# Optimization experiments

Hardware: AMD Instinct MI355X
Metric: run time of the kernel (lower is better)

Reference implementation:

```python
import jax, jax.numpy as jnp
import numpy as np

B, C, Himg, Wimg = 8, 256, 128, 128
KC, VC, HID = 256, 256, 1024


def _conv(x, w, b, pad, groups=1):
    y = jax.lax.conv_general_dilated(
        x, w, (1, 1), [(pad[0], pad[0]), (pad[1], pad[1])],
        dimension_numbers=('NCHW', 'OIHW', 'NCHW'), feature_group_count=groups)
    return y + b[None, :, None, None]


def _ln(x, g, b, eps=1e-5):
    m = x.mean(-1, keepdims=True)
    v = ((x - m) ** 2).mean(-1, keepdims=True)
    return (x - m) / jnp.sqrt(v + eps) * g + b


def setup_inputs() -> dict:
    key = jax.random.key(0)
    ks = jax.random.split(key, 24)
    s = 0.02
    inp = {
        'x': jax.random.normal(ks[0], (B, C, Himg, Wimg), jnp.float32),
        'H': Himg, 'W': Wimg,
        # directional K/Q convs: dir0 kernel (1,3), dir1 kernel (3,1)
        'wk1': s * jax.random.normal(ks[1], (KC, C, 1, 3), jnp.float32),
        'bk1': jnp.zeros((KC,), jnp.float32),
        'wk2': s * jax.random.normal(ks[2], (KC, C, 3, 1), jnp.float32),
        'bk2': jnp.zeros((KC,), jnp.float32),
        'wq1': s * jax.random.normal(ks[3], (KC, C, 1, 3), jnp.float32),
        'bq1': jnp.zeros((KC,), jnp.float32),
        'wq2': s * jax.random.normal(ks[4], (KC, C, 3, 1), jnp.float32),
        'bq2': jnp.zeros((KC,), jnp.float32),
        'wv': s * jax.random.normal(ks[5], (VC, C, 1, 1), jnp.float32),
        'bv': jnp.zeros((VC,), jnp.float32),
        'wr': s * jax.random.normal(ks[6], (C, 2 * VC, 1, 1), jnp.float32),
        'br': jnp.zeros((C,), jnp.float32),
        'g1': jnp.ones((C,), jnp.float32), 'b1': jnp.zeros((C,), jnp.float32),
        'g2': jnp.ones((C,), jnp.float32), 'b2': jnp.zeros((C,), jnp.float32),
        'w_fc1': s * jax.random.normal(ks[7], (HID, C), jnp.float32),
        'b_fc1': jnp.zeros((HID,), jnp.float32),
        'w_dw': s * jax.random.normal(ks[8], (HID, 1, 3, 3), jnp.float32),
        'b_dw': jnp.zeros((HID,), jnp.float32),
        'w_fc2': s * jax.random.normal(ks[9], (C, HID), jnp.float32),
        'b_fc2': jnp.zeros((C,), jnp.float32),
    }
    return inp


def reference(x, H, W, wk1, bk1, wk2, bk2, wq1, bq1, wq2, bq2, wv, bv, wr, br,
              g1, b1, g2, b2, w_fc1, b_fc1, w_dw, b_dw, w_fc2, b_fc2):
    b, c, h, w = x.shape
    N = h * w
    xseq = x.reshape(b, c, N).transpose(0, 2, 1)          # b N c
    n1 = _ln(xseq, g1, b1)
    xn = n1.transpose(0, 2, 1).reshape(b, c, h, w)

    val = _conv(xn, wv, bv, (0, 0)).reshape(b, VC, N)     # b vc n
    attended, maps = [], []
    ctx = None
    for (wk, bk, wq, bq, pad) in [(wk1, bk1, wq1, bq1, (0, 1)),
                                  (wk2, bk2, wq2, bq2, (1, 0))]:
        k = _conv(xn, wk, bk, pad).reshape(b, KC, N)
        q = _conv(xn, wq, bq, pad).reshape(b, KC, N)
        key_s = jax.nn.softmax(k, axis=2)                 # softmax over spatial
        qry_s = jax.nn.softmax(q, axis=1)                 # softmax over channels
        ctx = jnp.einsum('bkn,bvn->bkv', key_s, val)      # O(n) linear attention
        av = jnp.einsum('bkv,bkn->bvn', ctx, qry_s).reshape(b, VC, h, w)
        attended.append(av)
        maps.append(key_s.mean(axis=1).reshape(b, h, w))
    agg = jnp.concatenate(attended, axis=1)               # b 2vc h w
    attn = _conv(agg, wr, br, (0, 0))                     # b c h w
    amap = jnp.stack(maps, axis=0).mean(axis=0)

    tx = xseq + attn.reshape(b, c, N).transpose(0, 2, 1)  # residual
    n2 = _ln(tx, g2, b2)
    h1 = n2 @ w_fc1.T + b_fc1                             # b N 4c
    h1img = h1.transpose(0, 2, 1).reshape(b, HID, h, w)
    dw = _conv(h1img, w_dw, b_dw, (1, 1), groups=HID)
    a = jax.nn.gelu(dw.reshape(b, HID, N).transpose(0, 2, 1), approximate=False)
    ffn = a @ w_fc2.T + b_fc2
    mx = (tx + ffn).transpose(0, 2, 1).reshape(b, c, h, w)
    return (mx, ctx, amap)
```

## Files before the change

kernel.cpp:

```cpp
#include <hip/hip_runtime.h>
#include <hip/hip_bf16.h>

#define B_ 8
#define C_ 256
#define H_ 128
#define W_ 128
#define N_ 16384
#define KC_ 256
#define VC_ 256
#define HID_ 1024

typedef unsigned short ushort_t;
typedef __bf16 bf16x8 __attribute__((ext_vector_type(8)));
typedef float f32x4 __attribute__((ext_vector_type(4)));
typedef ushort_t u16x8 __attribute__((ext_vector_type(8)));

static __device__ __forceinline__ ushort_t f2bu(float f) {
  __hip_bfloat16 h = __float2bfloat16(f);
  return *reinterpret_cast<ushort_t*>(&h);
}
static __device__ __forceinline__ float bu2f(ushort_t u) {
  __hip_bfloat16 h;
  *reinterpret_cast<ushort_t*>(&h) = u;
  return __bfloat162float(h);
}

#define GLD16(gp, lp) __builtin_amdgcn_global_load_lds( \
    (const __attribute__((address_space(1))) void*)(gp), \
    (__attribute__((address_space(3))) void*)(lp), 16, 0, 0)

__global__ __launch_bounds__(256) void pack_all(
    const float* __restrict__ wk1, const float* __restrict__ wk2,
    const float* __restrict__ wq1, const float* __restrict__ wq2,
    const float* __restrict__ wv, const float* __restrict__ wfc1,
    const float* __restrict__ wfc2, const float* __restrict__ wdw,
    const float* __restrict__ bk1, const float* __restrict__ bk2,
    const float* __restrict__ bq1, const float* __restrict__ bq2,
    const float* __restrict__ bv, const float* __restrict__ wr,
    ushort_t* __restrict__ zbuf,
    float* __restrict__ bKV, float* __restrict__ bQ, float* __restrict__ wdwT,
    ushort_t* __restrict__ wvp, ushort_t* __restrict__ wfc1p,
    ushort_t* __restrict__ wfc2p, ushort_t* __restrict__ wrp,
    ushort_t* __restrict__ wkkp, ushort_t* __restrict__ wqqp) {
  int idx = blockIdx.x * 256 + threadIdx.x;
  const int MC = KC_ * C_;
  if (idx < 512) {
    zbuf[idx] = 0;
    bQ[idx] = (idx < 256) ? bq1[idx] : bq2[idx - 256];
    return;
  }
  idx -= 512;
  if (idx < 768) {
    bKV[idx] = (idx < 256) ? bk1[idx] : (idx < 512 ? bk2[idx - 256] : bv[idx - 512]);
    return;
  }
  idx -= 768;
  if (idx < 9216) { int c = idx / 9, t = idx % 9; wdwT[t * HID_ + c] = wdw[idx]; return; }
  idx -= 9216;
  if (idx < VC_ * C_) { wvp[idx] = f2bu(wv[idx]); return; }
  idx -= VC_ * C_;
  if (idx < HID_ * C_) { wfc1p[idx] = f2bu(wfc1[idx]); return; }
  idx -= HID_ * C_;
  if (idx < C_ * HID_) { wfc2p[idx] = f2bu(wfc2[idx]); return; }
  idx -= C_ * HID_;
  if (idx < C_ * 512) { wrp[idx] = f2bu(wr[idx]); return; }
  idx -= C_ * 512;
  if (idx < MC) {
    #pragma unroll
    for (int t = 0; t < 3; ++t) wkkp[t * MC + idx] = f2bu(wk1[idx * 3 + t]);
    return;
  }
  idx -= MC;
  if (idx < MC) {
    #pragma unroll
    for (int t = 0; t < 3; ++t) wkkp[3 * MC + t * MC + idx] = f2bu(wk2[idx * 3 + t]);
    return;
  }
  idx -= MC;
  if (idx < MC) {
    #pragma unroll
    for (int t = 0; t < 3; ++t) wqqp[t * MC + idx] = f2bu(wq1[idx * 3 + t]);
    return;
  }
  idx -= MC;
  if (idx < MC) {
    #pragma unroll
    for (int t = 0; t < 3; ++t) wqqp[3 * MC + t * MC + idx] = f2bu(wq2[idx * 3 + t]);
    return;
  }
}

__global__ __launch_bounds__(256) void ln1t_kernel(const float* __restrict__ x,
    const float* __restrict__ g, const float* __restrict__ beta,
    ushort_t* __restrict__ out) {
  __shared__ float T[256][67];
  __shared__ float st[2][4][64];
  __shared__ float mr[64], rs[64];
  int z = blockIdx.z;
  int n0 = blockIdx.x * 64;
  int t = threadIdx.x;
  const float* xb = x + (size_t)z * C_ * N_;
  #pragma unroll
  for (int j = 0; j < 16; ++j) {
    int e = (j * 256 + t) * 4;
    int c = e >> 6, n = e & 63;
    float4 v = *(const float4*)&xb[(size_t)c * N_ + n0 + n];
    T[c][n] = v.x; T[c][n + 1] = v.y; T[c][n + 2] = v.z; T[c][n + 3] = v.w;
  }
  __syncthreads();
  {
    int n = t & 63, part = t >> 6;
    float s1 = 0.f, s2 = 0.f;
    for (int c = part * 64; c < part * 64 + 64; ++c) { float v = T[c][n]; s1 += v; s2 += v * v; }
    st[0][part][n] = s1; st[1][part][n] = s2;
  }
  __syncthreads();
  if (t < 64) {
    float s1 = st[0][0][t] + st[0][1][t] + st[0][2][t] + st[0][3][t];
    float s2 = st[1][0][t] + st[1][1][t] + st[1][2][t] + st[1][3][t];
    float m = s1 * (1.f / C_);
    float v = s2 * (1.f / C_) - m * m;
    mr[t] = m; rs[t] = rsqrtf(v + 1e-5f);
  }
  __syncthreads();
  {
    int n = t >> 2, cc = (t & 3) * 64;
    float m = mr[n], r = rs[n];
    ushort_t* po = out + (size_t)z * N_ * C_ + (size_t)(n0 + n) * C_ + cc;
    #pragma unroll
    for (int j0 = 0; j0 < 64; j0 += 8) {
      u16x8 o;
      #pragma unroll
      for (int j = 0; j < 8; ++j) {
        int c = cc + j0 + j;
        o[j] = f2bu((T[c][n] - m) * r * g[c] + beta[c]);
      }
      *(u16x8*)(po + j0) = o;
    }
  }
}

__global__ __launch_bounds__(256) void ln2t_kernel(const ushort_t* __restrict__ x,
    const float* __restrict__ g, const float* __restrict__ beta,
    ushort_t* __restrict__ out) {
  __shared__ ushort_t T[256][72];
  __shared__ float st[2][4][64];
  __shared__ float mr[64], rs[64];
  int z = blockIdx.z;
  int n0 = blockIdx.x * 64;
  int t = threadIdx.x;
  const ushort_t* xb = x + (size_t)z * C_ * N_;
  #pragma unroll
  for (int j = 0; j < 8; ++j) {
    int e = (j * 256 + t) * 8;
    int c = e >> 6, n = e & 63;
    *(u16x8*)&T[c][n] = *(const u16x8*)&xb[(size_t)c * N_ + n0 + n];
  }
  __syncthreads();
  {
    int n = t & 63, part = t >> 6;
    float s1 = 0.f, s2 = 0.f;
    for (int c = part * 64; c < part * 64 + 64; ++c) { float v = bu2f(T[c][n]); s1 += v; s2 += v * v; }
    st[0][part][n] = s1; st[1][part][n] = s2;
  }
  __syncthreads();
  if (t < 64) {
    float s1 = st[0][0][t] + st[0][1][t] + st[0][2][t] + st[0][3][t];
    float s2 = st[1][0][t] + st[1][1][t] + st[1][2][t] + st[1][3][t];
    float m = s1 * (1.f / C_);
    float v = s2 * (1.f / C_) - m * m;
    mr[t] = m; rs[t] = rsqrtf(v + 1e-5f);
  }
  __syncthreads();
  {
    int n = t >> 2, cc = (t & 3) * 64;
    float m = mr[n], r = rs[n];
    ushort_t* po = out + (size_t)z * N_ * C_ + (size_t)(n0 + n) * C_ + cc;
    #pragma unroll
    for (int j0 = 0; j0 < 64; j0 += 8) {
      u16x8 o;
      #pragma unroll
      for (int j = 0; j < 8; ++j) {
        int c = cc + j0 + j;
        o[j] = f2bu((bu2f(T[c][n]) - m) * r * g[c] + beta[c]);
      }
      *(u16x8*)(po + j0) = o;
    }
  }
}

template<int TAPS, int DIMSEL, int OMODE, int SPLIT, bool BDUAL, bool BSOFT>
__global__ __launch_bounds__(256) void mfma_gemm(
    const ushort_t* __restrict__ A, long Abatch, int lda, long Aplane, long Adirstride,
    const ushort_t* __restrict__ B, const ushort_t* __restrict__ B2, long Bbatch, int ldb,
    const float* __restrict__ bias,
    const float* __restrict__ resF, const ushort_t* __restrict__ resB, long Resbatch,
    float* __restrict__ outF, ushort_t* __restrict__ outB, ushort_t* __restrict__ outB2,
    ushort_t* __restrict__ outB3,
    long Outbatch, int ldo, int Ksteps, const ushort_t* __restrict__ zbuf,
    const float2* __restrict__ qstats) {
  __shared__ ushort_t sm[17408];
  int tid = threadIdx.x;
  int bx = blockIdx.x, by = blockIdx.y, bz = blockIdx.z;
  if (gridDim.x == 128) bx = ((bx & 7) << 4) | (bx >> 3);
  int b = bz / SPLIT, sK = bz % SPLIT;
  long koff = (long)sK * Ksteps * 64;
  int dsel = (DIMSEL == 3) ? (by < 2 ? 1 : 2)
           : (DIMSEL == 4) ? (by < 2 ? 1 : (by < 4 ? 2 : 0))
           : DIMSEL;
  int m0 = (DIMSEL == 3 || DIMSEL == 4) ? ((by & 1) * 128) : (by * 128);
  int bofs = (DIMSEL == 3 || DIMSEL == 4) ? ((by >> 1) * 256) : 0;
  const ushort_t* Ab = A + (size_t)b * Abatch + koff
      + ((DIMSEL == 3 || DIMSEL == 4) ? (long)(by >> 1) * Adirstride : 0L);
  const ushort_t* Bb = B + (size_t)b * Bbatch + (BDUAL ? 0 : koff);
  const ushort_t* B2b = BDUAL ? (B2 + (size_t)b * Bbatch) : nullptr;
  int n0 = bx * 128;
  int lane = tid & 63, wid = tid >> 6, wm = wid >> 1, wn = wid & 1;

  f32x4 acc[4][4];
  #pragma unroll
  for (int i = 0; i < 4; i++)
    #pragma unroll
    for (int j = 0; j < 4; j++) acc[i][j] = (f32x4)0.f;

  for (int t = 0; t < TAPS; ++t) {
    if (TAPS == 3 && dsel == 2) {
      if ((bx == 0 && t == 0) || (bx == H_ - 1 && t == 2)) continue;
    }
    if (DIMSEL == 4 && dsel == 0 && t != 1) continue;
    const ushort_t* At = Ab + ((DIMSEL == 4 && dsel == 0) ? 0L : (long)t * Aplane);
    for (int ks = 0; ks < Ksteps; ++ks) {
      int k0 = ks * 64;
      #pragma unroll
      for (int i = 0; i < 4; i++) {
        int s = tid + i * 256;
        int row = s >> 3, pc = s & 7;
        int lc = pc ^ (row & 7);
        const ushort_t* g = At + (long)(m0 + row) * lda + k0 + lc * 8;
        GLD16(g, &sm[s * 8]);
      }
      if (BDUAL && BSOFT) {
        int dir = (ks < Ksteps / 2) ? 0 : 1;
        const ushort_t* Bsel = dir ? B2b : Bb;
        int kb = (ks - dir * (Ksteps / 2)) * 64;
        #pragma unroll
        for (int i = 0; i < 4; i++) {
          int s = tid + i * 256;
          int row = s >> 3, pc = s & 7;
          int lc = pc ^ (row & 7);
          u16x8 e = *(const u16x8*)(Bsel + (long)(n0 + row) * ldb + kb + lc * 8);
          float2 st = qstats[(size_t)dir * B_ * N_ + (size_t)bz * N_ + n0 + row];
          u16x8 o;
          #pragma unroll
          for (int j = 0; j < 8; j++)
            o[j] = f2bu(__expf(bu2f(e[j]) - st.x) * st.y);
          *(u16x8*)&sm[8192 + s * 8] = o;
        }
      } else {
        #pragma unroll
        for (int i = 0; i < 4; i++) {
          int s = tid + i * 256;
          int row = s >> 3, pc = s & 7;
          int lc = pc ^ (row & 7);
          const ushort_t* g;
          if (BDUAL) {
            const ushort_t* Bsel = (ks < Ksteps / 2) ? Bb : B2b;
            int kb = ((ks < Ksteps / 2) ? ks : ks - Ksteps / 2) * 64;
            g = Bsel + (long)(n0 + row) * ldb + kb + lc * 8;
          } else if (TAPS == 3 && dsel == 1) {
            int wpos = row + (t - 1);
            if (0 <= wpos && wpos < W_)
              g = Bb + (long)(n0 + row + (t - 1)) * ldb + k0 + lc * 8;
            else
              g = zbuf;
          } else if (TAPS == 3 && dsel == 2) {
            g = Bb + (long)(n0 + row + (t - 1) * W_) * ldb + k0 + lc * 8;
          } else {
            g = Bb + (long)(n0 + row) * ldb + k0 + lc * 8;
          }
          GLD16(g, &sm[8192 + s * 8]);
        }
      }
      __syncthreads();
      #pragma unroll
      for (int kk = 0; kk < 2; kk++) {
        bf16x8 av[4], bv[4];
        int r16 = lane & 15;
        int sl = (lane >> 4) + kk * 4;
        #pragma unroll
        for (int fm = 0; fm < 4; fm++) {
          int row = wm * 64 + fm * 16 + r16;
          av[fm] = *(const bf16x8*)&sm[row * 64 + ((sl ^ (row & 7)) * 8)];
        }
        #pragma unroll
        for (int fn = 0; fn < 4; fn++) {
          int row = wn * 64 + fn * 16 + r16;
          bv[fn] = *(const bf16x8*)&sm[8192 + row * 64 + ((sl ^ (row & 7)) * 8)];
        }
        #pragma unroll
        for (int fm = 0; fm < 4; fm++)
          #pragma unroll
          for (int fn = 0; fn < 4; fn++)
            acc[fm][fn] = __builtin_amdgcn_mfma_f32_16x16x32_bf16(av[fm], bv[fn], acc[fm][fn], 0, 0, 0);
      }
      __syncthreads();
    }
  }

  int r16 = lane & 15, rq = lane >> 4;
  if (OMODE == 1 || OMODE == 2 || OMODE == 7) {
    ushort_t* obase;
    if (DIMSEL == 3 || DIMSEL == 4)
      obase = (blockIdx.y >= 4) ? outB3 : (blockIdx.y >= 2 ? outB2 : outB);
    else
      obase = outB;
    ushort_t* ob = obase + (size_t)bz * Outbatch;
    #pragma unroll
    for (int fm = 0; fm < 4; fm++) {
      #pragma unroll
      for (int fn = 0; fn < 4; fn++) {
        int lm = wm * 64 + fm * 16 + rq * 4;
        int ln = wn * 64 + fn * 16 + r16;
        f32x4 a = acc[fm][fn];
        if (OMODE == 2) {
          #pragma unroll
          for (int r = 0; r < 4; r++)
            sm[ln * 136 + lm + r] = f2bu(a[r] + bias[bofs + m0 + lm + r]);
        } else {
          #pragma unroll
          for (int r = 0; r < 4; r++)
            sm[(lm + r) * 136 + ln] = f2bu(a[r] + bias[bofs + m0 + lm + r]);
        }
      }
    }
    __syncthreads();
    int row = tid >> 1, half = (tid & 1) * 64;
    const ushort_t* src = &sm[row * 136 + half];
    if (OMODE == 7) {
      const float* xb = resF + (size_t)bz * Resbatch + (size_t)(m0 + row) * ldo + n0 + half;
      ushort_t* dst = &ob[(size_t)(m0 + row) * ldo + n0 + half];
      #pragma unroll
      for (int j = 0; j < 8; j++) {
        u16x8 v = *(const u16x8*)(src + j * 8);
        float4 x0 = *(const float4*)(xb + j * 8);
        float4 x1 = *(const float4*)(xb + j * 8 + 4);
        u16x8 o;
        o[0] = f2bu(bu2f(v[0]) + x0.x); o[1] = f2bu(bu2f(v[1]) + x0.y);
        o[2] = f2bu(bu2f(v[2]) + x0.z); o[3] = f2bu(bu2f(v[3]) + x0.w);
        o[4] = f2bu(bu2f(v[4]) + x1.x); o[5] = f2bu(bu2f(v[5]) + x1.y);
        o[6] = f2bu(bu2f(v[6]) + x1.z); o[7] = f2bu(bu2f(v[7]) + x1.w);
        *(u16x8*)(dst + j * 8) = o;
      }
    } else {
      ushort_t* dst;
      if (OMODE == 1) dst = &ob[(size_t)(m0 + row) * ldo + n0 + half];
      else            dst = &ob[(size_t)(n0 + row) * ldo + m0 + half];
      #pragma unroll
      for (int j = 0; j < 8; j++)
        *(u16x8*)(dst + j * 8) = *(const u16x8*)(src + j * 8);
    }
  } else {
    #pragma unroll
    for (int fm = 0; fm < 4; fm++) {
      #pragma unroll
      for (int fn = 0; fn < 4; fn++) {
        int mrow = m0 + wm * 64 + fm * 16 + rq * 4;
        int ncol = n0 + wn * 64 + fn * 16 + r16;
        f32x4 a = acc[fm][fn];
        if (OMODE == 6) {
          float* of = outF + (size_t)bz * Outbatch;
          #pragma unroll
          for (int r = 0; r < 4; r++)
            of[(size_t)(mrow + r) * ldo + ncol] = a[r];
        } else if (OMODE == 8) {
          float* of = outF + (size_t)bz * Outbatch;
          const ushort_t* rp = resB + (size_t)bz * Resbatch;
          #pragma unroll
          for (int r = 0; r < 4; r++) {
            size_t o = (size_t)(mrow + r) * ldo + ncol;
            of[o] = a[r] + bias[mrow + r] + bu2f(rp[o]);
          }
        }
      }
    }
  }
}

__global__ __launch_bounds__(256) void softmax_spatial2(ushort_t* __restrict__ p0,
                                                        ushort_t* __restrict__ p1) {
  int r = blockIdx.x;
  ushort_t* p = (r < B_ * KC_) ? (p0 + (size_t)r * N_) : (p1 + (size_t)(r - B_ * KC_) * N_);
  int tid = threadIdx.x;
  __shared__ float red[256];
  u16x8 v[8];
  #pragma unroll
  for (int j = 0; j < 8; j++) v[j] = *(const u16x8*)&p[tid * 8 + j * 2048];
  float mx = -1e30f;
  #pragma unroll
  for (int j = 0; j < 8; j++)
    #pragma unroll
    for (int e = 0; e < 8; e++) mx = fmaxf(mx, bu2f(v[j][e]));
  red[tid] = mx; __syncthreads();
  for (int s = 128; s > 0; s >>= 1) { if (tid < s) red[tid] = fmaxf(red[tid], red[tid + s]); __syncthreads(); }
  mx = red[0]; __syncthreads();
  float sum = 0.f;
  #pragma unroll
  for (int j = 0; j < 8; j++)
    #pragma unroll
    for (int e = 0; e < 8; e++) sum += __expf(bu2f(v[j][e]) - mx);
  red[tid] = sum; __syncthreads();
  for (int s = 128; s > 0; s >>= 1) { if (tid < s) red[tid] += red[tid + s]; __syncthreads(); }
  float inv = 1.f / red[0];
  #pragma unroll
  for (int j = 0; j < 8; j++) {
    u16x8 o;
    #pragma unroll
    for (int e = 0; e < 8; e++) o[e] = f2bu(__expf(bu2f(v[j][e]) - mx) * inv);
    *(u16x8*)&p[tid * 8 + j * 2048] = o;
  }
}

__global__ __launch_bounds__(256) void chstats_kernel(const ushort_t* __restrict__ p0,
                                                      const ushort_t* __restrict__ p1,
                                                      float2* __restrict__ qstats) {
  int tid = threadIdx.x;
  size_t rowg = (size_t)blockIdx.x * 32 + (tid >> 3);
  int part = tid & 7;
  const ushort_t* q = (rowg < (size_t)B_ * N_) ? (p0 + rowg * KC_)
                                               : (p1 + (rowg - (size_t)B_ * N_) * KC_);
  u16x8 v[4];
  #pragma unroll
  for (int j = 0; j < 4; j++) v[j] = *(const u16x8*)&q[part * 8 + j * 64];
  float mx = -1e30f;
  #pragma unroll
  for (int j = 0; j < 4; j++)
    #pragma unroll
    for (int e = 0; e < 8; e++) mx = fmaxf(mx, bu2f(v[j][e]));
  mx = fmaxf(mx, __shfl_xor(mx, 1));
  mx = fmaxf(mx, __shfl_xor(mx, 2));
  mx = fmaxf(mx, __shfl_xor(mx, 4));
  float sum = 0.f;
  #pragma unroll
  for (int j = 0; j < 4; j++)
    #pragma unroll
    for (int e = 0; e < 8; e++) sum += __expf(bu2f(v[j][e]) - mx);
  sum += __shfl_xor(sum, 1);
  sum += __shfl_xor(sum, 2);
  sum += __shfl_xor(sum, 4);
  if (part == 0) qstats[rowg] = make_float2(mx, 1.f / sum);
}

__global__ __launch_bounds__(256) void amap2_kernel(const ushort_t* __restrict__ k0,
    const ushort_t* __restrict__ k1, float* __restrict__ amap) {
  __shared__ float red[256][8];
  int tid = threadIdx.x;
  int ngrp = tid & 63, part = tid >> 6;
  int nblock = blockIdx.x * 512;
  int b = nblock >> 14;
  int n = (nblock & 16383) + ngrp * 8;
  const ushort_t* b0 = k0 + (size_t)b * KC_ * N_ + n;
  const ushort_t* b1 = k1 + (size_t)b * KC_ * N_ + n;
  float s[8];
  #pragma unroll
  for (int j = 0; j < 8; j++) s[j] = 0.f;
  for (int c = part * 64; c < part * 64 + 64; ++c) {
    u16x8 a = *(const u16x8*)&b0[(size_t)c * N_];
    u16x8 d = *(const u16x8*)&b1[(size_t)c * N_];
    #pragma unroll
    for (int j = 0; j < 8; j++) s[j] += bu2f(a[j]) + bu2f(d[j]);
  }
  #pragma unroll
  for (int j = 0; j < 8; j++) red[tid][j] = s[j];
  __syncthreads();
  if (tid < 64) {
    float t[8];
    #pragma unroll
    for (int j = 0; j < 8; j++)
      t[j] = (red[tid][j] + red[tid + 64][j] + red[tid + 128][j] + red[tid + 192][j])
             * (1.f / (2.f * KC_));
    float* dst = amap + (size_t)nblock + tid * 8;
    *(float4*)dst = make_float4(t[0], t[1], t[2], t[3]);
    *(float4*)(dst + 4) = make_float4(t[4], t[5], t[6], t[7]);
  }
}

template<bool F32OUT>
__global__ __launch_bounds__(256) void ctx_reduce(const float* __restrict__ part,
                                                  float* __restrict__ outF,
                                                  ushort_t* __restrict__ outB, int split) {
  int idx = blockIdx.x * 256 + threadIdx.x;
  int b = idx >> 16;
  int r = idx & 65535;
  float s = 0.f;
  for (int k = 0; k < split; k++)
    s += part[((size_t)(b * split + k)) * KC_ * VC_ + r];
  if (F32OUT) outF[idx] = s;
  outB[idx] = f2bu(s);
}

__global__ __launch_bounds__(256) void dwgelu_t(const ushort_t* __restrict__ h1t,
    const float* __restrict__ wdwT, const float* __restrict__ bdw,
    ushort_t* __restrict__ actT) {
  const ushort_t* h1 = h1t + (size_t)blockIdx.y * N_ * HID_;
  ushort_t* act = actT + (size_t)blockIdx.y * N_ * HID_;
  int pix = blockIdx.x * 2 + (threadIdx.x >> 7);
  int c = (threadIdx.x & 127) * 8;
  int h = pix >> 7, w = pix & 127;
  float s[8];
  {
    float4 b0 = *(const float4*)&bdw[c];
    float4 b1 = *(const float4*)&bdw[c + 4];
    s[0]=b0.x; s[1]=b0.y; s[2]=b0.z; s[3]=b0.w;
    s[4]=b1.x; s[5]=b1.y; s[6]=b1.z; s[7]=b1.w;
  }
  #pragma unroll
  for (int di = -1; di <= 1; ++di) {
    int h2 = h + di;
    if ((unsigned)h2 >= H_) continue;
    #pragma unroll
    for (int dj = -1; dj <= 1; ++dj) {
      int w2 = w + dj;
      if ((unsigned)w2 >= W_) continue;
      int tap = (di + 1) * 3 + (dj + 1);
      u16x8 v = *(const u16x8*)&h1[(size_t)(h2 * W_ + w2) * HID_ + c];
      const float* wp = &wdwT[tap * HID_ + c];
      float4 w0 = *(const float4*)wp, w1 = *(const float4*)(wp + 4);
      s[0] += w0.x * bu2f(v[0]); s[1] += w0.y * bu2f(v[1]);
      s[2] += w0.z * bu2f(v[2]); s[3] += w0.w * bu2f(v[3]);
      s[4] += w1.x * bu2f(v[4]); s[5] += w1.y * bu2f(v[5]);
      s[6] += w1.z * bu2f(v[6]); s[7] += w1.w * bu2f(v[7]);
    }
  }
  u16x8 o;
  #pragma unroll
  for (int j = 0; j < 8; j++) {
    float gl = 0.5f * s[j] * (1.f + erff(s[j] * 0.70710678118654752f));
    o[j] = f2bu(gl);
  }
  *(u16x8*)&act[(size_t)pix * HID_ + c] = o;
}

extern "C" void kernel_launch(void* const* d_in, const int* in_sizes, int n_in,
                              void* d_out, int out_size, void* d_ws, size_t ws_size,
                              hipStream_t stream) {
  const float* x    = (const float*)d_in[0];
  const float* wk1  = (const float*)d_in[3];
  const float* bk1  = (const float*)d_in[4];
  const float* wk2  = (const float*)d_in[5];
  const float* bk2  = (const float*)d_in[6];
  const float* wq1  = (const float*)d_in[7];
  const float* bq1  = (const float*)d_in[8];
  const float* wq2  = (const float*)d_in[9];
  const float* bq2  = (const float*)d_in[10];
  const float* wv   = (const float*)d_in[11];
  const float* bv   = (const float*)d_in[12];
  const float* wr   = (const float*)d_in[13];
  const float* br   = (const float*)d_in[14];
  const float* g1   = (const float*)d_in[15];
  const float* b1   = (const float*)d_in[16];
  const float* g2   = (const float*)d_in[17];
  const float* b2   = (const float*)d_in[18];
  const float* wfc1 = (const float*)d_in[19];
  const float* bfc1 = (const float*)d_in[20];
  const float* wdw  = (const float*)d_in[21];
  const float* bdw  = (const float*)d_in[22];
  const float* wfc2 = (const float*)d_in[23];
  const float* bfc2 = (const float*)d_in[24];

  const size_t big = (size_t)B_ * C_ * N_;
  const long  CN  = (long)C_ * N_;
  const long  NC2 = (long)N_ * C_;
  const long  NH  = (long)N_ * HID_;
  const int   MC  = KC_ * C_;

  uint8_t* w8 = (uint8_t*)d_ws;
  size_t off = 0;
  ushort_t* xnt  = (ushort_t*)(w8 + off); off += 67108864;
  ushort_t* kq   = (ushort_t*)(w8 + off); off += 67108864;
  ushort_t* Mbuf = (ushort_t*)(w8 + off); off += (size_t)B_ * C_ * 512 * 2;
  ushort_t* wkkp = (ushort_t*)(w8 + off); off += 6 * MC * 2;
  ushort_t* wvp  = (ushort_t*)(w8 + off); off += MC * 2;
  ushort_t* wqqp = (ushort_t*)(w8 + off); off += 6 * MC * 2;
  ushort_t* wfc1p= (ushort_t*)(w8 + off); off += HID_ * C_ * 2;
  ushort_t* wfc2p= (ushort_t*)(w8 + off); off += C_ * HID_ * 2;
  float* wdwT    = (float*)(w8 + off);    off += 9 * HID_ * 4;
  float* bKV     = (float*)(w8 + off);    off += 768 * 4;
  float* bQ      = (float*)(w8 + off);    off += 512 * 4;
  ushort_t* wrp  = (ushort_t*)(w8 + off); off += C_ * 512 * 2;
  ushort_t* ctx0b= (ushort_t*)(w8 + off); off += (size_t)B_ * KC_ * VC_ * 2;
  ushort_t* ctx1b= (ushort_t*)(w8 + off); off += (size_t)B_ * KC_ * VC_ * 2;
  float2* qstats = (float2*)(w8 + off);   off += (size_t)2 * B_ * N_ * 8;
  ushort_t* zbuf = (ushort_t*)(w8 + off); off += 1024;
  const size_t partBytes = (size_t)8 * B_ * KC_ * VC_ * 4;
  size_t need_pair = off + 67108864 + partBytes;
  size_t need8 = off + partBytes;
  size_t need4 = off + partBytes / 2;
  int csplit; bool pairFFN = false;
  ushort_t* actX = nullptr;
  float* part;
  if (ws_size >= need_pair) {
    pairFFN = true; csplit = 8;
    actX = (ushort_t*)(w8 + off);
    part = (float*)(w8 + off + 67108864);
  } else if (ws_size >= need8) {
    csplit = 8; part = (float*)(w8 + off);
  } else if (ws_size >= need4) {
    csplit = 4; part = (float*)(w8 + off);
  } else return;
  const float* fzero = (const float*)zbuf;

  float* mx_out   = (float*)d_out;
  float* ctx_out  = mx_out + big;
  float* amap_out = ctx_out + (size_t)B_ * KC_ * VC_;

  ushort_t* mxlo = (ushort_t*)d_out;
  ushort_t* mxhi = (ushort_t*)d_out + big;

  ushort_t* txn  = xnt;

  dim3 blk(256);

  pack_all<<<3881, blk, 0, stream>>>(wk1, wk2, wq1, wq2, wv, wfc1, wfc2, wdw,
                                     bk1, bk2, bq1, bq2, bv, wr,
                                     zbuf, bKV, bQ, wdwT,
                                     wvp, wfc1p, wfc2p, wrp, wkkp, wqqp);

  ln1t_kernel<<<dim3(N_ / 64, 1, B_), blk, 0, stream>>>(x, g1, b1, xnt);

  mfma_gemm<3, 4, 1, 1, false, false><<<dim3(N_ / 128, 6, B_), blk, 0, stream>>>(
      wkkp, 0, C_, (long)MC, (long)3 * MC, xnt, nullptr, NC2, C_,
      bKV, nullptr, nullptr, 0,
      nullptr, kq, mxhi, mxlo, (long)KC_ * N_, N_, C_ / 64, zbuf, nullptr);

  softmax_spatial2<<<2 * B_ * KC_, blk, 0, stream>>>(kq, mxhi);
  amap2_kernel<<<B_ * N_ / 512, blk, 0, stream>>>(kq, mxhi, amap_out);

  for (int d = 0; d < 2; ++d) {
    const ushort_t* Ksrc = d ? mxhi : kq;
    if (csplit == 8)
      mfma_gemm<1, 0, 6, 8, false, false><<<dim3(VC_ / 128, KC_ / 128, B_ * 8), blk, 0, stream>>>(
          Ksrc, (long)KC_ * N_, N_, 0, 0, mxlo, nullptr, (long)VC_ * N_, N_,
          nullptr, nullptr, nullptr, 0,
          part, nullptr, nullptr, nullptr, (long)KC_ * VC_, VC_, (N_ / 8) / 64, zbuf, nullptr);
    else
      mfma_gemm<1, 0, 6, 4, false, false><<<dim3(VC_ / 128, KC_ / 128, B_ * 4), blk, 0, stream>>>(
          Ksrc, (long)KC_ * N_, N_, 0, 0, mxlo, nullptr, (long)VC_ * N_, N_,
          nullptr, nullptr, nullptr, 0,
          part, nullptr, nullptr, nullptr, (long)KC_ * VC_, VC_, (N_ / 4) / 64, zbuf, nullptr);
    if (d == 0)
      ctx_reduce<false><<<B_ * KC_ * VC_ / 256, blk, 0, stream>>>(part, nullptr, ctx0b, csplit);
    else
      ctx_reduce<true><<<B_ * KC_ * VC_ / 256, blk, 0, stream>>>(part, ctx_out, ctx1b, csplit);
  }

  mfma_gemm<3, 3, 2, 1, false, false><<<dim3(N_ / 128, 4, B_), blk, 0, stream>>>(
      wqqp, 0, C_, (long)MC, (long)3 * MC, xnt, nullptr, NC2, C_,
      bQ, nullptr, nullptr, 0,
      nullptr, kq, mxlo, nullptr, (long)N_ * KC_, KC_, C_ / 64, zbuf, nullptr);

  chstats_kernel<<<2 * B_ * N_ / 32, blk, 0, stream>>>(kq, mxlo, qstats);

  mfma_gemm<1, 0, 1, 1, false, false><<<dim3(KC_ / 128, C_ / 128, B_), blk, 0, stream>>>(
      wrp, 0, 512, 0, 0, ctx0b, nullptr, (long)KC_ * VC_, VC_, fzero, nullptr, nullptr, 0,
      nullptr, Mbuf, nullptr, nullptr, (long)C_ * 512, 512, VC_ / 64, zbuf, nullptr);
  mfma_gemm<1, 0, 1, 1, false, false><<<dim3(KC_ / 128, C_ / 128, B_), blk, 0, stream>>>(
      wrp + 256, 0, 512, 0, 0, ctx1b, nullptr, (long)KC_ * VC_, VC_, fzero, nullptr, nullptr, 0,
      nullptr, Mbuf + 256, nullptr, nullptr, (long)C_ * 512, 512, VC_ / 64, zbuf, nullptr);

  mfma_gemm<1, 0, 7, 1, true, true><<<dim3(N_ / 128, C_ / 128, B_), blk, 0, stream>>>(
      Mbuf, (long)C_ * 512, 512, 0, 0, kq, mxlo, (long)N_ * KC_, KC_,
      br, x, nullptr, CN,
      nullptr, mxhi, nullptr, nullptr, CN, N_, 8, zbuf, qstats);

  ln2t_kernel<<<dim3(N_ / 64, 1, B_), blk, 0, stream>>>(mxhi, g2, b2, txn);

  if (pairFFN) {
    hipMemcpyAsync(part, mxhi + (size_t)6 * CN, (size_t)2 * CN * 2,
                   hipMemcpyDeviceToDevice, stream);
    ushort_t* h1t2 = kq;
    for (int g = 0; g < 4; ++g) {
      mfma_gemm<1, 0, 2, 1, false, false><<<dim3(N_ / 128, HID_ / 128, 2), blk, 0, stream>>>(
          wfc1p, 0, C_, 0, 0, txn + (size_t)g * 2 * NC2, nullptr, NC2, C_,
          bfc1, nullptr, nullptr, 0,
          nullptr, h1t2, nullptr, nullptr, NH, HID_, C_ / 64, zbuf, nullptr);
      dwgelu_t<<<dim3(N_ / 2, 2), blk, 0, stream>>>(h1t2, wdwT, bdw, actX);
      const ushort_t* txb = (g == 3) ? (const ushort_t*)part : (mxhi + (size_t)g * 2 * CN);
      mfma_gemm<1, 0, 8, 1, false, false><<<dim3(N_ / 128, C_ / 128, 2), blk, 0, stream>>>(
          wfc2p, 0, HID_, 0, 0, actX, nullptr, NH, HID_,
          bfc2, nullptr, txb, CN,
          mx_out + (size_t)g * 2 * CN, nullptr, nullptr, nullptr, CN, N_, HID_ / 64, zbuf, nullptr);
    }
  } else {
    ushort_t* h1t  = kq;
    ushort_t* actT = kq + NH;
    hipMemcpyAsync(part, mxhi + (size_t)7 * CN, (size_t)CN * 2,
                   hipMemcpyDeviceToDevice, stream);
    for (int b = 0; b < B_; ++b) {
      mfma_gemm<1, 0, 2, 1, false, false><<<dim3(N_ / 128, HID_ / 128, 1), blk, 0, stream>>>(
          wfc1p, 0, C_, 0, 0, txn + (size_t)b * NC2, nullptr, 0, C_,
          bfc1, nullptr, nullptr, 0,
          nullptr, h1t, nullptr, nullptr, 0, HID_, C_ / 64, zbuf, nullptr);
      dwgelu_t<<<dim3(N_ / 2, 1), blk, 0, stream>>>(h1t, wdwT, bdw, actT);
      const ushort_t* txb = (b == 7) ? (const ushort_t*)part : (mxhi + (size_t)b * CN);
      mfma_gemm<1, 0, 8, 1, false, false><<<dim3(N_ / 128, C_ / 128, 1), blk, 0, stream>>>(
          wfc2p, 0, HID_, 0, 0, actT, nullptr, 0, HID_,
          bfc2, nullptr, txb, 0,
          mx_out + (size_t)b * CN, nullptr, nullptr, nullptr, 0, N_, HID_ / 64, zbuf, nullptr);
    }
  }
}
```

Before: 1.334 ms.

## Fuse Q channel stats into Q GEMM epilogue and batch both ctx directions

After: 1.287 ms (median of 3 runs). 1.04x faster.

```diff
diff --git a/kernel.cpp b/kernel.cpp
--- a/kernel.cpp
+++ b/kernel.cpp
@@ -189,19 +189,23 @@
   }
 }
 
-template<int TAPS, int DIMSEL, int OMODE, int SPLIT, bool BDUAL, bool BSOFT>
+template<int TAPS, int DIMSEL, int OMODE, int SPLIT, bool BDUAL, bool BSOFT, bool ADUAL, bool BSTATS>
 __global__ __launch_bounds__(256) void mfma_gemm(
-    const ushort_t* __restrict__ A, long Abatch, int lda, long Aplane, long Adirstride,
+    const ushort_t* __restrict__ A, const ushort_t* __restrict__ A2,
+    long Abatch, int lda, long Aplane, long Adirstride,
     const ushort_t* __restrict__ B, const ushort_t* __restrict__ B2, long Bbatch, int ldb,
     const float* __restrict__ bias,
     const float* __restrict__ resF, const ushort_t* __restrict__ resB, long Resbatch,
     float* __restrict__ outF, ushort_t* __restrict__ outB, ushort_t* __restrict__ outB2,
     ushort_t* __restrict__ outB3,
     long Outbatch, int ldo, int Ksteps, const ushort_t* __restrict__ zbuf,
-    const float2* __restrict__ qstats) {
+    const float2* __restrict__ qstats, float2* __restrict__ pstats, int adualH) {
   __shared__ ushort_t sm[17408];
   int tid = threadIdx.x;
-  int bx = blockIdx.x, by = blockIdx.y, bz = blockIdx.z;
+  int bx = blockIdx.x, by = blockIdx.y;
+  int bzfull = blockIdx.z;
+  bool adhi = ADUAL && (bzfull >= adualH);
+  int bz = adhi ? bzfull - adualH : bzfull;
   if (gridDim.x == 128) bx = ((bx & 7) << 4) | (bx >> 3);
   int b = bz / SPLIT, sK = bz % SPLIT;
   long koff = (long)sK * Ksteps * 64;
@@ -210,9 +214,11 @@
            : DIMSEL;
   int m0 = (DIMSEL == 3 || DIMSEL == 4) ? ((by & 1) * 128) : (by * 128);
   int bofs = (DIMSEL == 3 || DIMSEL == 4) ? ((by >> 1) * 256) : 0;
-  const ushort_t* Ab = A + (size_t)b * Abatch + koff
+  const ushort_t* Aroot = adhi ? A2 : A;
+  const ushort_t* Broot = (!BDUAL && adhi) ? B2 : B;
+  const ushort_t* Ab = Aroot + (size_t)b * Abatch + koff
       + ((DIMSEL == 3 || DIMSEL == 4) ? (long)(by >> 1) * Adirstride : 0L);
-  const ushort_t* Bb = B + (size_t)b * Bbatch + (BDUAL ? 0 : koff);
+  const ushort_t* Bb = Broot + (size_t)b * Bbatch + (BDUAL ? 0 : koff);
   const ushort_t* B2b = BDUAL ? (B2 + (size_t)b * Bbatch) : nullptr;
   int n0 = bx * 128;
   int lane = tid & 63, wid = tid >> 6, wm = wid >> 1, wn = wid & 1;
@@ -313,7 +319,7 @@
     if (DIMSEL == 3 || DIMSEL == 4)
       obase = (blockIdx.y >= 4) ? outB3 : (blockIdx.y >= 2 ? outB2 : outB);
     else
-      obase = outB;
+      obase = adhi ? outB2 : outB;
     ushort_t* ob = obase + (size_t)bz * Outbatch;
     #pragma unroll
     for (int fm = 0; fm < 4; fm++) {
@@ -359,6 +365,20 @@
       for (int j = 0; j < 8; j++)
         *(u16x8*)(dst + j * 8) = *(const u16x8*)(src + j * 8);
     }
+    if (OMODE == 2 && BSTATS) {
+      int colb = (tid & 1) * 64;
+      const ushort_t* rp = &sm[row * 136 + colb];
+      float mxl = -1e30f;
+      for (int j = 0; j < 64; ++j) mxl = fmaxf(mxl, bu2f(rp[j]));
+      float mxh = fmaxf(mxl, __shfl_xor(mxl, 1));
+      float s = 0.f;
+      for (int j = 0; j < 64; ++j) s += __expf(bu2f(rp[j]) - mxh);
+      s += __shfl_xor(s, 1);
+      if ((tid & 1) == 0) {
+        int dir = by >> 1, hlf = by & 1;
+        pstats[(((size_t)dir * B_ + bz) * N_ + n0 + row) * 2 + hlf] = make_float2(mxh, s);
+      }
+    }
   } else {
     #pragma unroll
     for (int fm = 0; fm < 4; fm++) {
@@ -368,7 +388,7 @@
         int ncol = n0 + wn * 64 + fn * 16 + r16;
         f32x4 a = acc[fm][fn];
         if (OMODE == 6) {
-          float* of = outF + (size_t)bz * Outbatch;
+          float* of = outF + (size_t)bzfull * Outbatch;
           #pragma unroll
           for (int r = 0; r < 4; r++)
             of[(size_t)(mrow + r) * ldo + ncol] = a[r];
@@ -403,11 +423,12 @@
   red[tid] = mx; __syncthreads();
   for (int s = 128; s > 0; s >>= 1) { if (tid < s) red[tid] = fmaxf(red[tid], red[tid + s]); __syncthreads(); }
   mx = red[0]; __syncthreads();
+  float ef[8][8];
   float sum = 0.f;
   #pragma unroll
   for (int j = 0; j < 8; j++)
     #pragma unroll
-    for (int e = 0; e < 8; e++) sum += __expf(bu2f(v[j][e]) - mx);
+    for (int e = 0; e < 8; e++) { ef[j][e] = __expf(bu2f(v[j][e]) - mx); sum += ef[j][e]; }
   red[tid] = sum; __syncthreads();
   for (int s = 128; s > 0; s >>= 1) { if (tid < s) red[tid] += red[tid + s]; __syncthreads(); }
   float inv = 1.f / red[0];
@@ -415,39 +436,19 @@
   for (int j = 0; j < 8; j++) {
     u16x8 o;
     #pragma unroll
-    for (int e = 0; e < 8; e++) o[e] = f2bu(__expf(bu2f(v[j][e]) - mx) * inv);
+    for (int e = 0; e < 8; e++) o[e] = f2bu(ef[j][e] * inv);
     *(u16x8*)&p[tid * 8 + j * 2048] = o;
   }
 }
 
-__global__ __launch_bounds__(256) void chstats_kernel(const ushort_t* __restrict__ p0,
-                                                      const ushort_t* __restrict__ p1,
-                                                      float2* __restrict__ qstats) {
-  int tid = threadIdx.x;
-  size_t rowg = (size_t)blockIdx.x * 32 + (tid >> 3);
-  int part = tid & 7;
-  const ushort_t* q = (rowg < (size_t)B_ * N_) ? (p0 + rowg * KC_)
-                                               : (p1 + (rowg - (size_t)B_ * N_) * KC_);
-  u16x8 v[4];
-  #pragma unroll
-  for (int j = 0; j < 4; j++) v[j] = *(const u16x8*)&q[part * 8 + j * 64];
-  float mx = -1e30f;
-  #pragma unroll
-  for (int j = 0; j < 4; j++)
-    #pragma unroll
-    for (int e = 0; e < 8; e++) mx = fmaxf(mx, bu2f(v[j][e]));
-  mx = fmaxf(mx, __shfl_xor(mx, 1));
-  mx = fmaxf(mx, __shfl_xor(mx, 2));
-  mx = fmaxf(mx, __shfl_xor(mx, 4));
-  float sum = 0.f;
-  #pragma unroll
-  for (int j = 0; j < 4; j++)
-    #pragma unroll
-    for (int e = 0; e < 8; e++) sum += __expf(bu2f(v[j][e]) - mx);
-  sum += __shfl_xor(sum, 1);
-  sum += __shfl_xor(sum, 2);
-  sum += __shfl_xor(sum, 4);
-  if (part == 0) qstats[rowg] = make_float2(mx, 1.f / sum);
+__global__ __launch_bounds__(256) void pcomb_kernel(const float2* __restrict__ pstats,
+                                                    float2* __restrict__ qstats) {
+  size_t idx = (size_t)blockIdx.x * 256 + threadIdx.x;
+  float2 a = pstats[idx * 2 + 0];
+  float2 b = pstats[idx * 2 + 1];
+  float mx = fmaxf(a.x, b.x);
+  float s = a.y * __expf(a.x - mx) + b.y * __expf(b.x - mx);
+  qstats[idx] = make_float2(mx, 1.f / s);
 }
 
 __global__ __launch_bounds__(256) void amap2_kernel(const ushort_t* __restrict__ k0,
@@ -484,18 +485,20 @@
   }
 }
 
-template<bool F32OUT>
-__global__ __launch_bounds__(256) void ctx_reduce(const float* __restrict__ part,
-                                                  float* __restrict__ outF,
-                                                  ushort_t* __restrict__ outB, int split) {
+__global__ __launch_bounds__(256) void ctx_reduce2(const float* __restrict__ part,
+                                                   float* __restrict__ ctxF,
+                                                   ushort_t* __restrict__ c0b,
+                                                   ushort_t* __restrict__ c1b) {
   int idx = blockIdx.x * 256 + threadIdx.x;
-  int b = idx >> 16;
-  int r = idx & 65535;
+  int dir = idx >> 19;
+  int rem = idx & 524287;
+  int b = rem >> 16;
+  const float* p = part + ((size_t)(dir * 64 + b * 8)) * 65536 + (rem & 65535);
   float s = 0.f;
-  for (int k = 0; k < split; k++)
-    s += part[((size_t)(b * split + k)) * KC_ * VC_ + r];
-  if (F32OUT) outF[idx] = s;
-  outB[idx] = f2bu(s);
+  #pragma unroll
+  for (int k = 0; k < 8; k++) s += p[(size_t)k * 65536];
+  if (dir == 0) c0b[rem] = f2bu(s);
+  else { ctxF[rem] = s; c1b[rem] = f2bu(s); }
 }
 
 __global__ __launch_bounds__(256) void dwgelu_t(const ushort_t* __restrict__ h1t,
@@ -590,22 +593,25 @@
   ushort_t* ctx0b= (ushort_t*)(w8 + off); off += (size_t)B_ * KC_ * VC_ * 2;
   ushort_t* ctx1b= (ushort_t*)(w8 + off); off += (size_t)B_ * KC_ * VC_ * 2;
   float2* qstats = (float2*)(w8 + off);   off += (size_t)2 * B_ * N_ * 8;
-  ushort_t* zbuf = (ushort_t*)(w8 + off); off += 1024;
-  const size_t partBytes = (size_t)8 * B_ * KC_ * VC_ * 4;
-  size_t need_pair = off + 67108864 + partBytes;
-  size_t need8 = off + partBytes;
-  size_t need4 = off + partBytes / 2;
-  int csplit; bool pairFFN = false;
+  float2* pstats = (float2*)(w8 + off);   off += (size_t)2 * B_ * N_ * 2 * 8;
+  ushort_t* zbuf = (ushort_t*)(w8 + off); off += 2048;
+  const size_t ctxpartBytes = (size_t)128 * KC_ * VC_ * 4;
+  const size_t txcopyBytes  = (size_t)2 * CN * 2;
+  size_t need_pair = off + 67108864 + txcopyBytes;
+  size_t need_np   = off + ctxpartBytes;
+  bool pairFFN;
   ushort_t* actX = nullptr;
-  float* part;
+  float* ctxpart;
+  ushort_t* txcopy;
   if (ws_size >= need_pair) {
-    pairFFN = true; csplit = 8;
+    pairFFN = true;
     actX = (ushort_t*)(w8 + off);
-    part = (float*)(w8 + off + 67108864);
-  } else if (ws_size >= need8) {
-    csplit = 8; part = (float*)(w8 + off);
-  } else if (ws_size >= need4) {
-    csplit = 4; part = (float*)(w8 + off);
+    ctxpart = (float*)(w8 + off);
+    txcopy = (ushort_t*)(w8 + off + 67108864);
+  } else if (ws_size >= need_np) {
+    pairFFN = false;
+    ctxpart = (float*)(w8 + off);
+    txcopy = (ushort_t*)(w8 + off);
   } else return;
   const float* fzero = (const float*)zbuf;
 
@@ -627,85 +633,75 @@
 
   ln1t_kernel<<<dim3(N_ / 64, 1, B_), blk, 0, stream>>>(x, g1, b1, xnt);
 
-  mfma_gemm<3, 4, 1, 1, false, false><<<dim3(N_ / 128, 6, B_), blk, 0, stream>>>(
-      wkkp, 0, C_, (long)MC, (long)3 * MC, xnt, nullptr, NC2, C_,
+  mfma_gemm<3, 4, 1, 1, false, false, false, false><<<dim3(N_ / 128, 6, B_), blk, 0, stream>>>(
+      wkkp, nullptr, 0, C_, (long)MC, (long)3 * MC, xnt, nullptr, NC2, C_,
       bKV, nullptr, nullptr, 0,
-      nullptr, kq, mxhi, mxlo, (long)KC_ * N_, N_, C_ / 64, zbuf, nullptr);
+      nullptr, kq, mxhi, mxlo, (long)KC_ * N_, N_, C_ / 64, zbuf, nullptr, nullptr, 0);
 
   softmax_spatial2<<<2 * B_ * KC_, blk, 0, stream>>>(kq, mxhi);
   amap2_kernel<<<B_ * N_ / 512, blk, 0, stream>>>(kq, mxhi, amap_out);
 
-  for (int d = 0; d < 2; ++d) {
-    const ushort_t* Ksrc = d ? mxhi : kq;
-    if (csplit == 8)
-      mfma_gemm<1, 0, 6, 8, false, false><<<dim3(VC_ / 128, KC_ / 128, B_ * 8), blk, 0, stream>>>(
-          Ksrc, (long)KC_ * N_, N_, 0, 0, mxlo, nullptr, (long)VC_ * N_, N_,
-          nullptr, nullptr, nullptr, 0,
-          part, nullptr, nullptr, nullptr, (long)KC_ * VC_, VC_, (N_ / 8) / 64, zbuf, nullptr);
-    else
-      mfma_gemm<1, 0, 6, 4, false, false><<<dim3(VC_ / 128, KC_ / 128, B_ * 4), blk, 0, stream>>>(
-          Ksrc, (long)KC_ * N_, N_, 0, 0, mxlo, nullptr, (long)VC_ * N_, N_,
-          nullptr, nullptr, nullptr, 0,
-          part, nullptr, nullptr, nullptr, (long)KC_ * VC_, VC_, (N_ / 4) / 64, zbuf, nullptr);
-    if (d == 0)
-      ctx_reduce<false><<<B_ * KC_ * VC_ / 256, blk, 0, stream>>>(part, nullptr, ctx0b, csplit);
-    else
-      ctx_reduce<true><<<B_ * KC_ * VC_ / 256, blk, 0, stream>>>(part, ctx_out, ctx1b, csplit);
-  }
-
-  mfma_gemm<3, 3, 2, 1, false, false><<<dim3(N_ / 128, 4, B_), blk, 0, stream>>>(
-      wqqp, 0, C_, (long)MC, (long)3 * MC, xnt, nullptr, NC2, C_,
+  mfma_gemm<1, 0, 6, 8, false, false, true, false><<<dim3(VC_ / 128, KC_ / 128, 128), blk, 0, stream>>>(
+      kq, mxhi, (long)KC_ * N_, N_, 0, 0, mxlo, mxlo, (long)VC_ * N_, N_,
+      nullptr, nullptr, nullptr, 0,
+      ctxpart, nullptr, nullptr, nullptr, (long)KC_ * VC_, VC_, (N_ / 8) / 64, zbuf,
+      nullptr, nullptr, 64);
+  ctx_reduce2<<<2 * B_ * KC_ * VC_ / 256, blk, 0, stream>>>(ctxpart, ctx_out, ctx0b, ctx1b);
+
+  mfma_gemm<3, 3, 2, 1, false, false, false, true><<<dim3(N_ / 128, 4, B_), blk, 0, stream>>>(
+      wqqp, nullptr, 0, C_, (long)MC, (long)3 * MC, xnt, nullptr, NC2, C_,
       bQ, nullptr, nullptr, 0,
-      nullptr, kq, mxlo, nullptr, (long)N_ * KC_, KC_, C_ / 64, zbuf, nullptr);
-
-  chstats_kernel<<<2 * B_ * N_ / 32, blk, 0, stream>>>(kq, mxlo, qstats);
-
-  mfma_gemm<1, 0, 1, 1, false, false><<<dim3(KC_ / 128, C_ / 128, B_), blk, 0, stream>>>(
-      wrp, 0, 512, 0, 0, ctx0b, nullptr, (long)KC_ * VC_, VC_, fzero, nullptr, nullptr, 0,
-      nullptr, Mbuf, nullptr, nullptr, (long)C_ * 512, 512, VC_ / 64, zbuf, nullptr);
-  mfma_gemm<1, 0, 1, 1, false, false><<<dim3(KC_ / 128, C_ / 128, B_), blk, 0, stream>>>(
-      wrp + 256, 0, 512, 0, 0, ctx1b, nullptr, (long)KC_ * VC_, VC_, fzero, nullptr, nullptr, 0,
-      nullptr, Mbuf + 256, nullptr, nullptr, (long)C_ * 512, 512, VC_ / 64, zbuf, nullptr);
-
-  mfma_gemm<1, 0, 7, 1, true, true><<<dim3(N_ / 128, C_ / 128, B_), blk, 0, stream>>>(
-      Mbuf, (long)C_ * 512, 512, 0, 0, kq, mxlo, (long)N_ * KC_, KC_,
+      nullptr, kq, mxlo, nullptr, (long)N_ * KC_, KC_, C_ / 64, zbuf, nullptr, pstats, 0);
+
+  pcomb_kernel<<<2 * B_ * N_ / 256, blk, 0, stream>>>(pstats, qstats);
+
+  mfma_gemm<1, 0, 2, 1, false, false, true, false><<<dim3(C_ / 128, KC_ / 128, 16), blk, 0, stream>>>(
+      ctx0b, ctx1b, (long)KC_ * VC_, VC_, 0, 0, wrp, wrp + 256, 0, 512,
+      fzero, nullptr, nullptr, 0,
+      nullptr, Mbuf, Mbuf + 256, nullptr, (long)C_ * 512, 512, VC_ / 64, zbuf,
+      nullptr, nullptr, 8);
+
+  mfma_gemm<1, 0, 7, 1, true, true, false, false><<<dim3(N_ / 128, C_ / 128, B_), blk, 0, stream>>>(
+      Mbuf, nullptr, (long)C_ * 512, 512, 0, 0, kq, mxlo, (long)N_ * KC_, KC_,
       br, x, nullptr, CN,
-      nullptr, mxhi, nullptr, nullptr, CN, N_, 8, zbuf, qstats);
+      nullptr, mxhi, nullptr, nullptr, CN, N_, 8, zbuf, qstats, nullptr, 0);
 
   ln2t_kernel<<<dim3(N_ / 64, 1, B_), blk, 0, stream>>>(mxhi, g2, b2, txn);
 
   if (pairFFN) {
-    hipMemcpyAsync(part, mxhi + (size_t)6 * CN, (size_t)2 * CN * 2,
+    hipMemcpyAsync(txcopy, mxhi + (size_t)6 * CN, (size_t)2 * CN * 2,
                    hipMemcpyDeviceToDevice, stream);
     ushort_t* h1t2 = kq;
     for (int g = 0; g < 4; ++g) {
-      mfma_gemm<1, 0, 2, 1, false, false><<<dim3(N_ / 128, HID_ / 128, 2), blk, 0, stream>>>(
-          wfc1p, 0, C_, 0, 0, txn + (size_t)g * 2 * NC2, nullptr, NC2, C_,
+      mfma_gemm<1, 0, 2, 1, false, false, false, false><<<dim3(N_ / 128, HID_ / 128, 2), blk, 0, stream>>>(
+          wfc1p, nullptr, 0, C_, 0, 0, txn + (size_t)g * 2 * NC2, nullptr, NC2, C_,
           bfc1, nullptr, nullptr, 0,
-          nullptr, h1t2, nullptr, nullptr, NH, HID_, C_ / 64, zbuf, nullptr);
+          nullptr, h1t2, nullptr, nullptr, NH, HID_, C_ / 64, zbuf, nullptr, nullptr, 0);
       dwgelu_t<<<dim3(N_ / 2, 2), blk, 0, stream>>>(h1t2, wdwT, bdw, actX);
-      const ushort_t* txb = (g == 3) ? (const ushort_t*)part : (mxhi + (size_t)g * 2 * CN);
-      mfma_gemm<1, 0, 8, 1, false, false><<<dim3(N_ / 128, C_ / 128, 2), blk, 0, stream>>>(
-          wfc2p, 0, HID_, 0, 0, actX, nullptr, NH, HID_,
+      const ushort_t* txb = (g == 3) ? (const ushort_t*)txcopy : (mxhi + (size_t)g * 2 * CN);
+      mfma_gemm<1, 0, 8, 1, false, false, false, false><<<dim3(N_ / 128, C_ / 128, 2), blk, 0, stream>>>(
+          wfc2p, nullptr, 0, HID_, 0, 0, actX, nullptr, NH, HID_,
           bfc2, nullptr, txb, CN,
-          mx_out + (size_t)g * 2 * CN, nullptr, nullptr, nullptr, CN, N_, HID_ / 64, zbuf, nullptr);
+          mx_out + (size_t)g * 2 * CN, nullptr, nullptr, nullptr, CN, N_, HID_ / 64, zbuf,
+          nullptr, nullptr, 0);
     }
   } else {
     ushort_t* h1t  = kq;
     ushort_t* actT = kq + NH;
-    hipMemcpyAsync(part, mxhi + (size_t)7 * CN, (size_t)CN * 2,
+    hipMemcpyAsync(txcopy, mxhi + (size_t)7 * CN, (size_t)CN * 2,
                    hipMemcpyDeviceToDevice, stream);
     for (int b = 0; b < B_; ++b) {
-      mfma_gemm<1, 0, 2, 1, false, false><<<dim3(N_ / 128, HID_ / 128, 1), blk, 0, stream>>>(
-          wfc1p, 0, C_, 0, 0, txn + (size_t)b * NC2, nullptr, 0, C_,
+      mfma_gemm<1, 0, 2, 1, false, false, false, false><<<dim3(N_ / 128, HID_ / 128, 1), blk, 0, stream>>>(
+          wfc1p, nullptr, 0, C_, 0, 0, txn + (size_t)b * NC2, nullptr, 0, C_,
           bfc1, nullptr, nullptr, 0,
-          nullptr, h1t, nullptr, nullptr, 0, HID_, C_ / 64, zbuf, nullptr);
+          nullptr, h1t, nullptr, nullptr, 0, HID_, C_ / 64, zbuf, nullptr, nullptr, 0);
       dwgelu_t<<<dim3(N_ / 2, 1), blk, 0, stream>>>(h1t, wdwT, bdw, actT);
-      const ushort_t* txb = (b == 7) ? (const ushort_t*)part : (mxhi + (size_t)b * CN);
-      mfma_gemm<1, 0, 8, 1, false, false><<<dim3(N_ / 128, C_ / 128, 1), blk, 0, stream>>>(
-          wfc2p, 0, HID_, 0, 0, actT, nullptr, 0, HID_,
+      const ushort_t* txb = (b == 7) ? (const ushort_t*)txcopy : (mxhi + (size_t)b * CN);
+      mfma_gemm<1, 0, 8, 1, false, false, false, false><<<dim3(N_ / 128, C_ / 128, 1), blk, 0, stream>>>(
+          wfc2p, nullptr, 0, HID_, 0, 0, actT, nullptr, 0, HID_,
           bfc2, nullptr, txb, 0,
-          mx_out + (size_t)b * CN, nullptr, nullptr, nullptr, 0, N_, HID_ / 64, zbuf, nullptr);
-    }
-  }
-}
+          mx_out + (size_t)b * CN, nullptr, nullptr, nullptr, 0, N_, HID_ / 64, zbuf,
+          nullptr, nullptr, 0);
+    }
+  }
+}
```
